# Kernel tuning notes

Measured on AMD Instinct MI355X. Metric: run time of the kernel, lower is better.

Reference implementation:

```python
import jax, jax.numpy as jnp
import numpy as np


def setup_inputs() -> dict:
    key = jax.random.key(0)
    k1, k2 = jax.random.split(key)
    _input = jax.random.normal(k1, (64, 8, 256, 256), dtype=jnp.float32)
    _filter = jax.random.normal(k2, (8, 8, 3, 3), dtype=jnp.float32)
    return {"_input": _input, "_filter": _filter}


def reference(_input, _filter):
    # The original module builds an im2col buffer with Python loops and does a
    # single GEMM; the math is exactly a stride-1, VALID-padding cross-correlation:
    #   out[n,m,i,j] = sum_{c,r,s} input[n,c,i+r,j+s] * filter[m,c,r,s]
    # Expressed as the efficient implicit-GEMM convolution primitive.
    out = jax.lax.conv_general_dilated(
        _input, _filter,
        window_strides=(1, 1),
        padding="VALID",
        dimension_numbers=("NCHW", "OIHW", "NCHW"),
    )
    return out  # (N, M, H-R+1, W-S+1)
```

## Files before the change

### kernel.cpp

```cpp
#include <hip/hip_runtime.h>


#define XW 66
#define ROWS 18

typedef _Float16 half8 __attribute__((ext_vector_type(8)));
typedef float floatx4 __attribute__((ext_vector_type(4)));

__global__ __launch_bounds__(256, 4)
void conv2d_mfma_kernel(const float* __restrict__ inp,
                        const float* __restrict__ filt,
                        float* __restrict__ out) {
    __shared__ __align__(16) _Float16 s_in[ROWS * XW * 8];

    const int tid = threadIdx.x;
    const int x0 = blockIdx.x * 64;
    const int y0 = blockIdx.y * 16;
    const int n  = blockIdx.z;

    const float* in_n = inp + (size_t)n * (8 * 256 * 256);

    #pragma unroll
    for (int it = 0; it < 5; ++it) {
        int cell = tid + it * 256;
        if (cell < ROWS * XW) {
            int row = cell / XW;
            int col = cell - row * XW;
            int iy = y0 + row;
            int ix = x0 + col;
            bool ok = (iy < 256) && (ix < 256);
            const float* p = in_n + (iy * 256 + ix);
            half8 h;
            #pragma unroll
            for (int c = 0; c < 8; ++c) {
                float v = ok ? p[c * 65536] : 0.0f;
                h[c] = (_Float16)v;
            }
            *reinterpret_cast<half8*>(&s_in[cell * 8]) = h;
        }
    }

    const int lane = tid & 63;
    const int w    = tid >> 6;
    const int lx   = lane & 15;
    const int g    = lane >> 4;

    half8 afrag[3];
    int   dcell[3];
    #pragma unroll
    for (int kk = 0; kk < 3; ++kk) {
        int q  = kk * 4 + g;
        int qa = q > 8 ? 8 : q;
        int r  = qa / 3;
        int s  = qa - r * 3;
        dcell[kk] = r * XW + s;
        half8 a = {};
        if (q <= 8 && lx < 8) {
            #pragma unroll
            for (int j = 0; j < 8; ++j)
                a[j] = (_Float16)filt[lx * 72 + j * 9 + q];
        }
        afrag[kk] = a;
    }

    __syncthreads();

    #pragma unroll
    for (int yy = 0; yy < 4; ++yy) {
        const int y = w * 4 + yy;
        const int rowbase = y * XW + lx;
        #pragma unroll
        for (int xg = 0; xg < 4; ++xg) {
            floatx4 acc = {0.0f, 0.0f, 0.0f, 0.0f};
            #pragma unroll
            for (int kk = 0; kk < 3; ++kk) {
                const half8 b = *reinterpret_cast<const half8*>(
                    &s_in[(rowbase + xg * 16 + dcell[kk]) * 8]);
                acc = __builtin_amdgcn_mfma_f32_16x16x32_f16(
                          afrag[kk], b, acc, 0, 0, 0);
            }
            const int ox = x0 + xg * 16 + lx;
            const int oy = y0 + y;
            if (g < 2 && oy < 254 && ox < 254) {
                #pragma unroll
                for (int i = 0; i < 4; ++i) {
                    const int m = g * 4 + i;
                    out[(((size_t)n * 8 + m) * 254 + oy) * 254 + ox] = acc[i];
                }
            }
        }
    }
}

extern "C" void kernel_launch(void* const* d_in, const int* in_sizes, int n_in,
                              void* d_out, int out_size, void* d_ws, size_t ws_size,
                              hipStream_t stream) {
    const float* inp  = (const float*)d_in[0];
    const float* filt = (const float*)d_in[1];
    float* outp = (float*)d_out;

    dim3 grid(4, 16, 64);
    dim3 block(256);
    conv2d_mfma_kernel<<<grid, block, 0, stream>>>(inp, filt, outp);
}
```

Baseline: 303.3 us.

## Process four row tiles per block with double-buffered LDS and register prefetch

```diff
diff --git a/kernel.cpp b/kernel.cpp
--- a/kernel.cpp
+++ b/kernel.cpp
@@ -3,6 +3,7 @@
 
 #define XW 66
 #define ROWS 18
+#define CELLS (ROWS * XW)
 
 typedef _Float16 half8 __attribute__((ext_vector_type(8)));
 typedef float floatx4 __attribute__((ext_vector_type(4)));
@@ -11,34 +12,44 @@
 void conv2d_mfma_kernel(const float* __restrict__ inp,
                         const float* __restrict__ filt,
                         float* __restrict__ out) {
-    __shared__ __align__(16) _Float16 s_in[ROWS * XW * 8];
+    __shared__ __align__(16) _Float16 s_in[2][CELLS * 8];
 
     const int tid = threadIdx.x;
-    const int x0 = blockIdx.x * 64;
-    const int y0 = blockIdx.y * 16;
-    const int n  = blockIdx.z;
+    const int x0     = blockIdx.x * 64;
+    const int ystrip = blockIdx.y * 64;
+    const int n      = blockIdx.z;
 
-    const float* in_n = inp + (size_t)n * (8 * 256 * 256);
+    const float* in_n  = inp + (size_t)n * (8 * 256 * 256);
+    float*       out_n = out + (size_t)n * (8 * 254 * 254);
 
+    int  srow[5], sgx[5];
+    bool sok[5];
     #pragma unroll
-    for (int it = 0; it < 5; ++it) {
-        int cell = tid + it * 256;
-        if (cell < ROWS * XW) {
-            int row = cell / XW;
-            int col = cell - row * XW;
-            int iy = y0 + row;
-            int ix = x0 + col;
-            bool ok = (iy < 256) && (ix < 256);
-            const float* p = in_n + (iy * 256 + ix);
-            half8 h;
+    for (int i = 0; i < 5; ++i) {
+        int  idx = tid + i * 256;
+        bool act = idx < CELLS;
+        int  ci  = act ? idx : 0;
+        srow[i] = ci / XW;
+        int col = ci - srow[i] * XW;
+        sgx[i]  = x0 + col;
+        sok[i]  = act && (sgx[i] < 256);
+    }
+
+    float v[5][8];
+    auto issue_loads = [&](int t) {
+        const int ybase = ystrip + t * 16;
+        #pragma unroll
+        for (int i = 0; i < 5; ++i) {
+            const int  iy = ybase + srow[i];
+            const bool ok = sok[i] && (iy < 256);
+            const float* p = in_n + iy * 256 + sgx[i];
             #pragma unroll
-            for (int c = 0; c < 8; ++c) {
-                float v = ok ? p[c * 65536] : 0.0f;
-                h[c] = (_Float16)v;
-            }
-            *reinterpret_cast<half8*>(&s_in[cell * 8]) = h;
+            for (int c = 0; c < 8; ++c)
+                v[i][c] = ok ? p[c * 65536] : 0.0f;
         }
-    }
+    };
+
+    issue_loads(0);
 
     const int lane = tid & 63;
     const int w    = tid >> 6;
@@ -52,8 +63,8 @@
         int q  = kk * 4 + g;
         int qa = q > 8 ? 8 : q;
         int r  = qa / 3;
-        int s  = qa - r * 3;
-        dcell[kk] = r * XW + s;
+        int s2 = qa - r * 3;
+        dcell[kk] = r * XW + s2;
         half8 a = {};
         if (q <= 8 && lx < 8) {
             #pragma unroll
@@ -63,29 +74,53 @@
         afrag[kk] = a;
     }
 
-    __syncthreads();
+    #pragma unroll
+    for (int t = 0; t < 4; ++t) {
+        const int s = t & 1;
 
-    #pragma unroll
-    for (int yy = 0; yy < 4; ++yy) {
-        const int y = w * 4 + yy;
-        const int rowbase = y * XW + lx;
         #pragma unroll
-        for (int xg = 0; xg < 4; ++xg) {
-            floatx4 acc = {0.0f, 0.0f, 0.0f, 0.0f};
+        for (int i = 0; i < 5; ++i) {
+            if (i < 4 || tid < CELLS - 1024) {
+                half8 h;
+                #pragma unroll
+                for (int c = 0; c < 8; ++c) h[c] = (_Float16)v[i][c];
+                *reinterpret_cast<half8*>(&s_in[s][(tid + i * 256) * 8]) = h;
+            }
+        }
+        __syncthreads();
+
+        if (t < 3) {
+            issue_loads(t + 1);
+            __builtin_amdgcn_sched_barrier(0);
+        }
+
+        #pragma unroll
+        for (int yy = 0; yy < 4; ++yy) {
+            const int y       = w * 4 + yy;
+            const int rowbase = y * XW + lx;
+            floatx4 acc[4] = {{0,0,0,0},{0,0,0,0},{0,0,0,0},{0,0,0,0}};
             #pragma unroll
             for (int kk = 0; kk < 3; ++kk) {
-                const half8 b = *reinterpret_cast<const half8*>(
-                    &s_in[(rowbase + xg * 16 + dcell[kk]) * 8]);
-                acc = __builtin_amdgcn_mfma_f32_16x16x32_f16(
-                          afrag[kk], b, acc, 0, 0, 0);
+                #pragma unroll
+                for (int xg = 0; xg < 4; ++xg) {
+                    const half8 b = *reinterpret_cast<const half8*>(
+                        &s_in[s][(rowbase + xg * 16 + dcell[kk]) * 8]);
+                    acc[xg] = __builtin_amdgcn_mfma_f32_16x16x32_f16(
+                                  afrag[kk], b, acc[xg], 0, 0, 0);
+                }
             }
-            const int ox = x0 + xg * 16 + lx;
-            const int oy = y0 + y;
-            if (g < 2 && oy < 254 && ox < 254) {
+            const int oy = ystrip + t * 16 + y;
+            if (g < 2 && oy < 254) {
+                const int offy = oy * 254;
                 #pragma unroll
-                for (int i = 0; i < 4; ++i) {
-                    const int m = g * 4 + i;
-                    out[(((size_t)n * 8 + m) * 254 + oy) * 254 + ox] = acc[i];
+                for (int xg = 0; xg < 4; ++xg) {
+                    const int ox = x0 + xg * 16 + lx;
+                    if (ox < 254) {
+                        float* op = out_n + (g * 4) * 64516 + offy + ox;
+                        #pragma unroll
+                        for (int i = 0; i < 4; ++i)
+                            op[i * 64516] = acc[xg][i];
+                    }
                 }
             }
         }
@@ -99,7 +134,7 @@
     const float* filt = (const float*)d_in[1];
     float* outp = (float*)d_out;
 
-    dim3 grid(4, 16, 64);
+    dim3 grid(4, 4, 64);
     dim3 block(256);
     conv2d_mfma_kernel<<<grid, block, 0, stream>>>(inp, filt, outp);
 }
```

Measured after the change: 309.2 us. About the same (+2.0%).

## Stream full-width row chunks through a triple-buffered LDS ring per block

Applied to the files above, without the earlier changes.

```diff
diff --git a/kernel.cpp b/kernel.cpp
--- a/kernel.cpp
+++ b/kernel.cpp
@@ -1,44 +1,23 @@
 #include <hip/hip_runtime.h>
 
 
-#define XW 66
-#define ROWS 18
+#define SLOT_HALFS (4 * 256 * 8)
 
 typedef _Float16 half8 __attribute__((ext_vector_type(8)));
 typedef float floatx4 __attribute__((ext_vector_type(4)));
 
-__global__ __launch_bounds__(256, 4)
+__global__ __launch_bounds__(256, 3)
 void conv2d_mfma_kernel(const float* __restrict__ inp,
                         const float* __restrict__ filt,
                         float* __restrict__ out) {
-    __shared__ __align__(16) _Float16 s_in[ROWS * XW * 8];
+    __shared__ __align__(16) _Float16 s_in[3 * SLOT_HALFS + 64];
 
-    const int tid = threadIdx.x;
-    const int x0 = blockIdx.x * 64;
-    const int y0 = blockIdx.y * 16;
-    const int n  = blockIdx.z;
+    const int tid    = threadIdx.x;
+    const int ystrip = blockIdx.x * 32;
+    const int n      = blockIdx.y;
 
-    const float* in_n = inp + (size_t)n * (8 * 256 * 256);
-
-    #pragma unroll
-    for (int it = 0; it < 5; ++it) {
-        int cell = tid + it * 256;
-        if (cell < ROWS * XW) {
-            int row = cell / XW;
-            int col = cell - row * XW;
-            int iy = y0 + row;
-            int ix = x0 + col;
-            bool ok = (iy < 256) && (ix < 256);
-            const float* p = in_n + (iy * 256 + ix);
-            half8 h;
-            #pragma unroll
-            for (int c = 0; c < 8; ++c) {
-                float v = ok ? p[c * 65536] : 0.0f;
-                h[c] = (_Float16)v;
-            }
-            *reinterpret_cast<half8*>(&s_in[cell * 8]) = h;
-        }
-    }
+    const float* in_n  = inp + (size_t)n * (8 * 256 * 256);
+    float*       out_n = out + (size_t)n * (8 * 254 * 254);
 
     const int lane = tid & 63;
     const int w    = tid >> 6;
@@ -46,14 +25,13 @@
     const int g    = lane >> 4;
 
     half8 afrag[3];
-    int   dcell[3];
+    int roff[3], soff[3];
     #pragma unroll
     for (int kk = 0; kk < 3; ++kk) {
         int q  = kk * 4 + g;
         int qa = q > 8 ? 8 : q;
-        int r  = qa / 3;
-        int s  = qa - r * 3;
-        dcell[kk] = r * XW + s;
+        roff[kk] = qa / 3;
+        soff[kk] = qa - roff[kk] * 3;
         half8 a = {};
         if (q <= 8 && lx < 8) {
             #pragma unroll
@@ -63,32 +41,70 @@
         afrag[kk] = a;
     }
 
+    float v[4][8];
+    auto load_chunk = [&](int ck) {
+        #pragma unroll
+        for (int k = 0; k < 4; ++k) {
+            const int  iy = ystrip + ck * 4 + k;
+            const bool ok = iy < 256;
+            const float* p = in_n + iy * 256 + tid;
+            #pragma unroll
+            for (int c = 0; c < 8; ++c)
+                v[k][c] = ok ? p[c * 65536] : 0.0f;
+        }
+    };
+    auto write_chunk = [&](int ck) {
+        _Float16* base = &s_in[(ck % 3) * SLOT_HALFS];
+        #pragma unroll
+        for (int k = 0; k < 4; ++k) {
+            half8 h;
+            #pragma unroll
+            for (int c = 0; c < 8; ++c) h[c] = (_Float16)v[k][c];
+            *reinterpret_cast<half8*>(&base[(k * 256 + tid) * 8]) = h;
+        }
+    };
+
+    load_chunk(0); write_chunk(0);
+    load_chunk(1); write_chunk(1);
     __syncthreads();
 
-    #pragma unroll
-    for (int yy = 0; yy < 4; ++yy) {
-        const int y = w * 4 + yy;
-        const int rowbase = y * XW + lx;
+    for (int t = 0; t < 8; ++t) {
+        if (t < 7) load_chunk(t + 2);
+
+        const int ro = t * 4 + w;
+        const int oy = ystrip + ro;
+
+        const _Float16* bptr[3];
         #pragma unroll
-        for (int xg = 0; xg < 4; ++xg) {
+        for (int kk = 0; kk < 3; ++kk) {
+            int L    = ro + roff[kk];
+            int slot = (L >> 2) % 3;
+            bptr[kk] = &s_in[slot * SLOT_HALFS +
+                             ((L & 3) * 256 + lx + soff[kk]) * 8];
+        }
+
+        const bool do_store = (g < 2) && (oy < 254);
+        #pragma unroll
+        for (int xg = 0; xg < 16; ++xg) {
             floatx4 acc = {0.0f, 0.0f, 0.0f, 0.0f};
             #pragma unroll
             for (int kk = 0; kk < 3; ++kk) {
-                const half8 b = *reinterpret_cast<const half8*>(
-                    &s_in[(rowbase + xg * 16 + dcell[kk]) * 8]);
+                const half8 b =
+                    *reinterpret_cast<const half8*>(bptr[kk] + xg * 128);
                 acc = __builtin_amdgcn_mfma_f32_16x16x32_f16(
                           afrag[kk], b, acc, 0, 0, 0);
             }
-            const int ox = x0 + xg * 16 + lx;
-            const int oy = y0 + y;
-            if (g < 2 && oy < 254 && ox < 254) {
+            const int ox = xg * 16 + lx;
+            if (do_store && ox < 254) {
+                float* op = out_n + (g * 4) * 64516 + oy * 254 + ox;
                 #pragma unroll
-                for (int i = 0; i < 4; ++i) {
-                    const int m = g * 4 + i;
-                    out[(((size_t)n * 8 + m) * 254 + oy) * 254 + ox] = acc[i];
-                }
+                for (int i = 0; i < 4; ++i)
+                    op[i * 64516] = acc[i];
             }
         }
+
+        if (t < 7) write_chunk(t + 2);
+        __syncthreads();
     }
 }
 
@@ -99,7 +115,7 @@
     const float* filt = (const float*)d_in[1];
     float* outp = (float*)d_out;
 
-    dim3 grid(4, 16, 64);
+    dim3 grid(8, 64, 1);
     dim3 block(256);
     conv2d_mfma_kernel<<<grid, block, 0, stream>>>(inp, filt, outp);
 }
```

Result: no change. 306.8 us (+1.2%).
